# Performance work log

Measured on AMD Instinct MI355X. Metric: run time of the kernel, lower is better.

## Reference

```python
import jax, jax.numpy as jnp
import numpy as np

B, M, H, D, C = 512, 40, 128, 64, 128


def setup_inputs() -> dict:
    key = jax.random.key(0)
    k1, k2, k3, k4 = jax.random.split(key, 4)
    x0 = jax.random.normal(k1, (B, M, D), dtype=jnp.float32)
    xk = jax.random.normal(k2, (B, H, D), dtype=jnp.float32)
    # Conv1d(kernel_size=1) weight [C, H*M, 1] squeezed to [C, H*M]; bias [C]
    W = jax.random.normal(k3, (C, H * M), dtype=jnp.float32) * 0.02
    b = jax.random.normal(k4, (C,), dtype=jnp.float32) * 0.02
    return {"x0": x0, "xk": xk, "W": W, "b": b}


def reference(x0, xk, W, b):
    # torch: outer[b, h*M+m, d] = xk[b,h,d] * x0[b,m,d]; out = conv1d(outer)
    # conv1d with kernel_size=1 is a channel contraction:
    #   out[b,c,d] = sum_{h,m} W[c, h*M+m] * xk[b,h,d] * x0[b,m,d] + b[c]
    Bsz, Hh, Dd = xk.shape
    Mm = x0.shape[1]
    Cc = W.shape[0]
    Wr = W.reshape(Cc, Hh, Mm)  # channel index is h*M + m -> [C, H, M]
    out = jnp.einsum('bhd,bmd,chm->bcd', xk, x0, Wr) + b[None, :, None]
    return out  # [B, C, D]
```

## Files before the change

### kernel.cpp

```cpp
#include <hip/hip_runtime.h>
#include <hip/hip_bf16.h>

typedef __attribute__((ext_vector_type(8))) short short8;
typedef __attribute__((ext_vector_type(4))) float f32x4;
typedef unsigned short u16;
typedef unsigned int u32;

#define NB 512
#define NM 40
#define NH 128
#define ND 64
#define NC 128
#define KTOT 5120

__device__ __forceinline__ u16 f2bf_rne(float f) {
    u32 u = __float_as_uint(f);
    u32 r = u + 0x7FFFu + ((u >> 16) & 1u);
    return (u16)(r >> 16);
}

__global__ void w3_kernel(const float* __restrict__ W, u16* __restrict__ W3) {
    __shared__ u16 kbuf[KTOT];
    const int c = blockIdx.x;
    const float* src = W + (size_t)c * KTOT;
    for (int k = threadIdx.x; k < KTOT; k += 256)
        kbuf[k] = f2bf_rne(src[k]);
    __syncthreads();
    for (int n = threadIdx.x; n < 640; n += 256) {
        int m = n >> 4, t = (n >> 2) & 3, q = n & 3;
        union { short8 s8; u16 e[8]; } v;
#pragma unroll
        for (int j = 0; j < 8; ++j)
            v.e[j] = kbuf[(t * 32 + q * 8 + j) * NM + m];
        *(short8*)(W3 + ((size_t)n * 128 + c) * 8) = v.s8;
    }
}

__global__ void __launch_bounds__(512, 2) cin_main(
    const float* __restrict__ x0g, const float* __restrict__ xkg,
    const float* __restrict__ biasg, const u16* __restrict__ W3,
    float* __restrict__ out)
{
    __shared__ __align__(16) char smem[70144];
    short* xkT    = (short*)smem;
    float* x0s    = (float*)(smem + 34816);
    float* red    = (float*)smem;
    float* bias_s = (float*)(smem + 69632);

    const int tid = threadIdx.x;
    const int w = tid >> 6, L = tid & 63;
    const int q = L >> 4, l16 = L & 15;
    const int bh = (w >> 2) & 1;
    const int rh = (w >> 1) & 1;
    const int mh = w & 1;
    const size_t b0 = 2 * (size_t)blockIdx.x;

    const u16* Ap = W3 + q * 1024 + (size_t)(rh * 64 + l16) * 8;
    const int m0 = mh * 20;

    short8 aP[2][4];
    auto loadAstep = [&](int u, short8* dst) {
        const size_t m = (size_t)(m0 + (u >> 2));
        const int t = u & 3;
        const u16* p = Ap + m * 16384 + t * 4096;
#pragma unroll
        for (int mt = 0; mt < 4; ++mt)
            dst[mt] = *(const short8*)(p + mt * 128);
    };
    loadAstep(0, aP[0]);
    loadAstep(1, aP[1]);

    {
        for (int i = tid; i < 4096; i += 512) {
            int bn = i >> 11, rem = i & 2047;
            int h = rem >> 4, d4 = (rem & 15) << 2;
            float4 v = *(const float4*)(xkg + (b0 + bn) * (NH * ND) + h * ND + d4);
            short* xT = xkT + bn * 8704;
            xT[(d4 + 0) * 136 + h] = (short)f2bf_rne(v.x);
            xT[(d4 + 1) * 136 + h] = (short)f2bf_rne(v.y);
            xT[(d4 + 2) * 136 + h] = (short)f2bf_rne(v.z);
            xT[(d4 + 3) * 136 + h] = (short)f2bf_rne(v.w);
        }
        for (int i = tid; i < 1280; i += 512) {
            int bn = i / 640, rem = i % 640;
            int m = rem >> 4, d4 = (rem & 15) << 2;
            *(f32x4*)(x0s + bn * 2720 + m * 68 + d4) =
                *(const f32x4*)(x0g + (b0 + bn) * (NM * ND) + m * ND + d4);
        }
        if (tid < NC) bias_s[tid] = biasg[tid];
    }
    __syncthreads();

    const short* xT = xkT + bh * 8704;
    const float* x0p = x0s + bh * 2720;
    const short* Bp = xT + (size_t)l16 * 136 + q * 8;
    short8 bR[4][4];
#pragma unroll
    for (int t = 0; t < 4; ++t)
#pragma unroll
        for (int n = 0; n < 4; ++n)
            bR[t][n] = *(const short8*)(Bp + n * (16 * 136) + t * 32);

    float s[4], sn[4];
#pragma unroll
    for (int n = 0; n < 4; ++n)
        s[n] = x0p[m0 * 68 + n * 16 + l16];

    f32x4 T[4][4] = {};
    f32x4 o[4][4] = {};

#pragma unroll 4
    for (int u = 0; u < 80; ++u) {
        const int t = u & 3;
        short8* aC = aP[u & 1];
        if (t == 0) {
            const int m = m0 + (u >> 2);
#pragma unroll
            for (int n = 0; n < 4; ++n)
                sn[n] = ((u >> 2) < 19) ? x0p[(m + 1) * 68 + n * 16 + l16] : 0.f;
        }
#pragma unroll
        for (int n = 0; n < 4; ++n) {
            T[0][n] = __builtin_amdgcn_mfma_f32_16x16x32_bf16(aC[0], bR[t][n], T[0][n], 0, 0, 0);
            T[1][n] = __builtin_amdgcn_mfma_f32_16x16x32_bf16(aC[1], bR[t][n], T[1][n], 0, 0, 0);
            T[2][n] = __builtin_amdgcn_mfma_f32_16x16x32_bf16(aC[2], bR[t][n], T[2][n], 0, 0, 0);
            T[3][n] = __builtin_amdgcn_mfma_f32_16x16x32_bf16(aC[3], bR[t][n], T[3][n], 0, 0, 0);
        }
        const int up = (u + 2 < 80) ? (u + 2) : u;
        loadAstep(up, aC);
        if (t == 3) {
#pragma unroll
            for (int n = 0; n < 4; ++n) {
                const float dd = s[n] - sn[n];
#pragma unroll
                for (int mt = 0; mt < 4; ++mt)
                    o[mt][n] += dd * T[mt][n];
                s[n] = sn[n];
            }
        }
    }

    __syncthreads();
    float* myred = red + (bh * 2 + rh) * 4352;
    if (mh == 1) {
#pragma unroll
        for (int mt = 0; mt < 4; ++mt)
#pragma unroll
            for (int n = 0; n < 4; ++n) {
                int d = n * 16 + l16;
                *(f32x4*)(myred + d * 68 + mt * 16 + q * 4) = o[mt][n];
            }
    }
    __syncthreads();
    if (mh == 0) {
        float* op = out + (b0 + bh) * (NC * ND);
#pragma unroll
        for (int mt = 0; mt < 4; ++mt)
#pragma unroll
            for (int n = 0; n < 4; ++n) {
                int d = n * 16 + l16;
                f32x4 r = *(const f32x4*)(myred + d * 68 + mt * 16 + q * 4);
#pragma unroll
                for (int rr = 0; rr < 4; ++rr) {
                    int c = rh * 64 + mt * 16 + q * 4 + rr;
                    op[c * ND + d] = o[mt][n][rr] + r[rr] + bias_s[c];
                }
            }
    }
}

extern "C" void kernel_launch(void* const* d_in, const int* in_sizes, int n_in,
                              void* d_out, int out_size, void* d_ws, size_t ws_size,
                              hipStream_t stream) {
    const float* x0 = (const float*)d_in[0];
    const float* xk = (const float*)d_in[1];
    const float* W  = (const float*)d_in[2];
    const float* bi = (const float*)d_in[3];
    float* out = (float*)d_out;

    u16* W3 = (u16*)d_ws;

    w3_kernel<<<NC, 256, 0, stream>>>(W, W3);
    cin_main<<<NB / 2, 512, 0, stream>>>(x0, xk, bi, W3, out);
}
```

Baseline: 115.9 us.

## Assign one batch per block with each wave owning 16 output channels

The main kernel now processes one batch element per block instead of two. Each of the 8 waves owns a 16-channel slice and runs over all 40 m values, so the split-m reduction through shared memory and its extra barriers go away. LDS use and per-wave register tiles shrink, which may raise occupancy and the grid doubles to 512 blocks. The cost is that each W3 fragment loaded from global/L2 now feeds only 4 MFMAs instead of 16, so weight traffic per FLOP rises, and the loop runs twice as many serial steps.

```diff
diff --git a/kernel.cpp b/kernel.cpp
--- a/kernel.cpp
+++ b/kernel.cpp
@@ -41,59 +41,47 @@
     const float* __restrict__ biasg, const u16* __restrict__ W3,
     float* __restrict__ out)
 {
-    __shared__ __align__(16) char smem[70144];
+    __shared__ __align__(16) char smem[28800];
     short* xkT    = (short*)smem;
-    float* x0s    = (float*)(smem + 34816);
-    float* red    = (float*)smem;
-    float* bias_s = (float*)(smem + 69632);
+    float* x0s    = (float*)(smem + 17408);
+    float* bias_s = (float*)(smem + 28288);
 
     const int tid = threadIdx.x;
     const int w = tid >> 6, L = tid & 63;
     const int q = L >> 4, l16 = L & 15;
-    const int bh = (w >> 2) & 1;
-    const int rh = (w >> 1) & 1;
-    const int mh = w & 1;
-    const size_t b0 = 2 * (size_t)blockIdx.x;
+    const size_t b = blockIdx.x;
 
-    const u16* Ap = W3 + q * 1024 + (size_t)(rh * 64 + l16) * 8;
-    const int m0 = mh * 20;
+    const u16* Ap = W3 + q * 1024 + (size_t)(w * 16 + l16) * 8;
 
-    short8 aP[2][4];
+    short8 aP[2];
     auto loadAstep = [&](int u, short8* dst) {
-        const size_t m = (size_t)(m0 + (u >> 2));
+        const size_t m = (size_t)(u >> 2);
         const int t = u & 3;
-        const u16* p = Ap + m * 16384 + t * 4096;
-#pragma unroll
-        for (int mt = 0; mt < 4; ++mt)
-            dst[mt] = *(const short8*)(p + mt * 128);
+        *dst = *(const short8*)(Ap + m * 16384 + t * 4096);
     };
-    loadAstep(0, aP[0]);
-    loadAstep(1, aP[1]);
+    loadAstep(0, &aP[0]);
+    loadAstep(1, &aP[1]);
 
     {
-        for (int i = tid; i < 4096; i += 512) {
-            int bn = i >> 11, rem = i & 2047;
-            int h = rem >> 4, d4 = (rem & 15) << 2;
-            float4 v = *(const float4*)(xkg + (b0 + bn) * (NH * ND) + h * ND + d4);
-            short* xT = xkT + bn * 8704;
-            xT[(d4 + 0) * 136 + h] = (short)f2bf_rne(v.x);
-            xT[(d4 + 1) * 136 + h] = (short)f2bf_rne(v.y);
-            xT[(d4 + 2) * 136 + h] = (short)f2bf_rne(v.z);
-            xT[(d4 + 3) * 136 + h] = (short)f2bf_rne(v.w);
+        const float* xp = xkg + b * (NH * ND);
+        for (int i = tid; i < 2048; i += 512) {
+            int h = i >> 4, d4 = (i & 15) << 2;
+            float4 v = *(const float4*)(xp + h * ND + d4);
+            xkT[(d4 + 0) * 136 + h] = (short)f2bf_rne(v.x);
+            xkT[(d4 + 1) * 136 + h] = (short)f2bf_rne(v.y);
+            xkT[(d4 + 2) * 136 + h] = (short)f2bf_rne(v.z);
+            xkT[(d4 + 3) * 136 + h] = (short)f2bf_rne(v.w);
         }
-        for (int i = tid; i < 1280; i += 512) {
-            int bn = i / 640, rem = i % 640;
-            int m = rem >> 4, d4 = (rem & 15) << 2;
-            *(f32x4*)(x0s + bn * 2720 + m * 68 + d4) =
-                *(const f32x4*)(x0g + (b0 + bn) * (NM * ND) + m * ND + d4);
+        const float* x0p = x0g + b * (NM * ND);
+        for (int i = tid; i < 640; i += 512) {
+            int m = i >> 4, d4 = (i & 15) << 2;
+            *(f32x4*)(x0s + m * 68 + d4) = *(const f32x4*)(x0p + m * ND + d4);
         }
         if (tid < NC) bias_s[tid] = biasg[tid];
     }
     __syncthreads();
 
-    const short* xT = xkT + bh * 8704;
-    const float* x0p = x0s + bh * 2720;
-    const short* Bp = xT + (size_t)l16 * 136 + q * 8;
+    const short* Bp = xkT + (size_t)l16 * 136 + q * 8;
     short8 bR[4][4];
 #pragma unroll
     for (int t = 0; t < 4; ++t)
@@ -104,68 +92,45 @@
     float s[4], sn[4];
 #pragma unroll
     for (int n = 0; n < 4; ++n)
-        s[n] = x0p[m0 * 68 + n * 16 + l16];
+        s[n] = x0s[n * 16 + l16];
 
-    f32x4 T[4][4] = {};
-    f32x4 o[4][4] = {};
+    f32x4 T[4] = {};
+    f32x4 o[4] = {};
 
 #pragma unroll 4
-    for (int u = 0; u < 80; ++u) {
+    for (int u = 0; u < 160; ++u) {
         const int t = u & 3;
-        short8* aC = aP[u & 1];
         if (t == 0) {
-            const int m = m0 + (u >> 2);
+            const int m = u >> 2;
 #pragma unroll
             for (int n = 0; n < 4; ++n)
-                sn[n] = ((u >> 2) < 19) ? x0p[(m + 1) * 68 + n * 16 + l16] : 0.f;
+                sn[n] = (m < 39) ? x0s[(m + 1) * 68 + n * 16 + l16] : 0.f;
         }
+        const short8 aC = aP[u & 1];
 #pragma unroll
-        for (int n = 0; n < 4; ++n) {
-            T[0][n] = __builtin_amdgcn_mfma_f32_16x16x32_bf16(aC[0], bR[t][n], T[0][n], 0, 0, 0);
-            T[1][n] = __builtin_amdgcn_mfma_f32_16x16x32_bf16(aC[1], bR[t][n], T[1][n], 0, 0, 0);
-            T[2][n] = __builtin_amdgcn_mfma_f32_16x16x32_bf16(aC[2], bR[t][n], T[2][n], 0, 0, 0);
-            T[3][n] = __builtin_amdgcn_mfma_f32_16x16x32_bf16(aC[3], bR[t][n], T[3][n], 0, 0, 0);
-        }
-        const int up = (u + 2 < 80) ? (u + 2) : u;
-        loadAstep(up, aC);
+        for (int n = 0; n < 4; ++n)
+            T[n] = __builtin_amdgcn_mfma_f32_16x16x32_bf16(aC, bR[t][n], T[n], 0, 0, 0);
+        const int up = (u + 2 < 160) ? (u + 2) : u;
+        loadAstep(up, &aP[u & 1]);
         if (t == 3) {
 #pragma unroll
             for (int n = 0; n < 4; ++n) {
                 const float dd = s[n] - sn[n];
-#pragma unroll
-                for (int mt = 0; mt < 4; ++mt)
-                    o[mt][n] += dd * T[mt][n];
+                o[n] += dd * T[n];
                 s[n] = sn[n];
             }
         }
     }
 
-    __syncthreads();
-    float* myred = red + (bh * 2 + rh) * 4352;
-    if (mh == 1) {
+    float* op = out + b * (NC * ND);
 #pragma unroll
-        for (int mt = 0; mt < 4; ++mt)
+    for (int n = 0; n < 4; ++n) {
+        const int d = n * 16 + l16;
 #pragma unroll
-            for (int n = 0; n < 4; ++n) {
-                int d = n * 16 + l16;
-                *(f32x4*)(myred + d * 68 + mt * 16 + q * 4) = o[mt][n];
-            }
-    }
-    __syncthreads();
-    if (mh == 0) {
-        float* op = out + (b0 + bh) * (NC * ND);
-#pragma unroll
-        for (int mt = 0; mt < 4; ++mt)
-#pragma unroll
-            for (int n = 0; n < 4; ++n) {
-                int d = n * 16 + l16;
-                f32x4 r = *(const f32x4*)(myred + d * 68 + mt * 16 + q * 4);
-#pragma unroll
-                for (int rr = 0; rr < 4; ++rr) {
-                    int c = rh * 64 + mt * 16 + q * 4 + rr;
-                    op[c * ND + d] = o[mt][n][rr] + r[rr] + bias_s[c];
-                }
-            }
+        for (int rr = 0; rr < 4; ++rr) {
+            const int c = w * 16 + q * 4 + rr;
+            op[c * ND + d] = o[n][rr] + bias_s[c];
+        }
     }
 }
 
@@ -181,5 +146,5 @@
     u16* W3 = (u16*)d_ws;
 
     w3_kernel<<<NC, 256, 0, stream>>>(W, W3);
-    cin_main<<<NB / 2, 512, 0, stream>>>(x0, xk, bi, W3, out);
+    cin_main<<<NB, 512, 0, stream>>>(x0, xk, bi, W3, out);
 }
```

Result: slower. 130.7 us (+12.7%).
